# Kernel optimization log

Hardware: AMD Instinct MI355X
Metric: run time of the kernel (lower is better)

## Reference

```python
import jax, jax.numpy as jnp
import numpy as np

B, L, C = 32, 4096, 64
PL, PC = 64, 16          # patch sizes along L and C
NP = 256                 # num_patches
OUT = 512                # output_dim
FS = 1000.0              # sampling frequency -> T = 1/FS


def setup_inputs() -> dict:
    key = jax.random.key(0)
    ks = jax.random.split(key, 7)
    d_in = PL * (PC * 2)
    return {
        "x": jax.random.normal(ks[0], (B, L, C), dtype=jnp.float32),
        "start_L": jax.random.randint(ks[1], (B, NP), 0, L - PL + 1, dtype=jnp.int32),
        "start_C": jax.random.randint(ks[2], (B, NP), 0, C - PC + 1, dtype=jnp.int32),
        "w1": jax.random.normal(ks[3], (OUT, d_in), dtype=jnp.float32) / np.sqrt(d_in),
        "b1": jax.random.normal(ks[4], (OUT,), dtype=jnp.float32) * 0.01,
        "w2": jax.random.normal(ks[5], (OUT, OUT), dtype=jnp.float32) / np.sqrt(OUT),
        "b2": jax.random.normal(ks[6], (OUT,), dtype=jnp.float32) * 0.01,
    }


def reference(x, start_L, start_C, w1, b1, w2, b2):
    T = 1.0 / FS
    t = jnp.arange(L, dtype=jnp.float32) * T                      # [L]

    # patch index grids (wrapping, as in the torch module)
    idx_L = (start_L[:, :, None] + jnp.arange(PL, dtype=jnp.int32)) % L   # [B,NP,PL]
    idx_C = (start_C[:, :, None] + jnp.arange(PC, dtype=jnp.int32)) % C   # [B,NP,PC]

    # double gather: patches[b,p,i,j] = x[b, idx_L[b,p,i], idx_C[b,p,j]]
    b_idx = jnp.arange(B, dtype=jnp.int32)[:, None, None, None]
    patches = x[b_idx, idx_L[:, :, :, None], idx_C[:, :, None, :]]        # [B,NP,PL,PC]

    # time embedding gathered with the same L indices, broadcast over PC
    t_patches = jnp.broadcast_to(t[idx_L][:, :, :, None], (B, NP, PL, PC))

    feats = jnp.concatenate([patches, t_patches], axis=-1)                # [B,NP,PL,2*PC]
    feats = feats.reshape(B, NP, PL * 2 * PC)

    h = jnp.einsum('bpd,od->bpo', feats, w1) + b1
    h = jax.nn.silu(h)
    out = jnp.einsum('bpo,qo->bpq', h, w2) + b2                           # [B,NP,OUT]
    return out
```

## Files before the change

kernel.cpp:

```cpp
#include <hip/hip_runtime.h>
#include <hip/hip_bf16.h>
#include <stdint.h>

#define BB   32
#define LL   4096
#define CCH  64
#define NPp  256
#define DOUT 512
#define DINX 1024
#define MM   (BB * NPp)
#define TT   0.001f

using bf16 = __hip_bfloat16;
typedef __attribute__((ext_vector_type(8))) short bf16x8;
typedef __attribute__((ext_vector_type(4))) float f32x4;

__device__ __forceinline__ void async_copy16(void* lds, const void* g) {
    __builtin_amdgcn_global_load_lds(
        (const __attribute__((address_space(1))) void*)g,
        (__attribute__((address_space(3))) void*)lds,
        16, 0, 0);
}

__device__ __forceinline__ uint2 pack4_bf16(float a, float b, float c, float d) {
    union { bf16 h[4]; uint2 u; } p;
    p.h[0] = __float2bfloat16(a);
    p.h[1] = __float2bfloat16(b);
    p.h[2] = __float2bfloat16(c);
    p.h[3] = __float2bfloat16(d);
    return p.u;
}

__global__ __launch_bounds__(256) void prep(
    const float* __restrict__ w1, const float* __restrict__ b1,
    const float* __restrict__ w2,
    bf16* __restrict__ w1x, bf16* __restrict__ w2b,
    float* __restrict__ A1, float* __restrict__ C1)
{
    const int blk = blockIdx.x;
    if (blk < 512) {
        int i = (blk * 256 + threadIdx.x) * 4;
        int o = i >> 10, r = i & 1023;
        int l = r >> 4, j = r & 15;
        float4 v = *(const float4*)(w1 + (size_t)o * 2048 + l * 32 + j);
        *(uint2*)(w1x + i) = pack4_bf16(v.x, v.y, v.z, v.w);
    } else if (blk < 768) {
        int i = ((blk - 512) * 256 + threadIdx.x) * 4;
        float4 v = *(const float4*)(w2 + i);
        *(uint2*)(w2b + i) = pack4_bf16(v.x, v.y, v.z, v.w);
    } else {
        const int o = (blk - 768) * 4 + (threadIdx.x >> 6);
        const int l = threadIdx.x & 63;
        const float* wr = w1 + (size_t)o * 2048 + l * 32 + 16;
        float s0 = 0.f;
#pragma unroll
        for (int j = 0; j < 16; ++j) s0 += wr[j];
        float s1 = (float)l * s0;
#pragma unroll
        for (int off = 32; off > 0; off >>= 1) {
            s0 += __shfl_down(s0, off);
            s1 += __shfl_down(s1, off);
        }
        if (l == 0) {
            A1[o] = TT * s0;
            C1[o] = b1[o] + TT * s1;
        }
    }
}

__global__ __launch_bounds__(256) void gather_feats(
    const float* __restrict__ x, const int* __restrict__ startL,
    const int* __restrict__ startC, bf16* __restrict__ feats)
{
    const int m = blockIdx.x * 4 + (threadIdx.x >> 6);
    const int b = m >> 8;
    const int l = threadIdx.x & 63;
    const int sl = startL[m];
    const int sc = startC[m];
    const float* src = x + ((size_t)b * LL + (size_t)(sl + l)) * CCH + sc;
    float4 v0 = *(const float4*)(src);
    float4 v1 = *(const float4*)(src + 4);
    float4 v2 = *(const float4*)(src + 8);
    float4 v3 = *(const float4*)(src + 12);
    uint4 p0, p1;
    uint2 a = pack4_bf16(v0.x, v0.y, v0.z, v0.w);
    uint2 c = pack4_bf16(v1.x, v1.y, v1.z, v1.w);
    p0.x = a.x; p0.y = a.y; p0.z = c.x; p0.w = c.y;
    a = pack4_bf16(v2.x, v2.y, v2.z, v2.w);
    c = pack4_bf16(v3.x, v3.y, v3.z, v3.w);
    p1.x = a.x; p1.y = a.y; p1.z = c.x; p1.w = c.y;
    bf16* dst = feats + (size_t)m * DINX + l * 16;
    *(uint4*)dst       = p0;
    *(uint4*)(dst + 8) = p1;
}

template <bool FUSE1>
__global__ __launch_bounds__(256, 4) void gemm_db(
    const bf16* __restrict__ A,
    const bf16* __restrict__ Bt,
    const float* __restrict__ P1,
    const float* __restrict__ C1,
    const int*   __restrict__ sL,
    void* __restrict__ outp,
    const int N, const int K)
{
    constexpr int BK = 64;
    __shared__ __align__(16) bf16 As[2][64 * BK];
    __shared__ __align__(16) bf16 Bs[2][64 * BK];

    const int tid  = threadIdx.x;
    const int lane = tid & 63;
    const int wave = tid >> 6;
    const int row0 = blockIdx.x * 64;
    const int col0 = blockIdx.y * 64;

    const int  srow  = wave * 16 + (lane >> 3);
    const int  skoff = (lane & 7) * 8;
    const bf16* agp = A  + (size_t)(row0 + srow) * K + skoff;
    const bf16* bgp = Bt + (size_t)(col0 + srow) * K + skoff;
    const int w16 = wave * 16;

    const int mw = (wave >> 1) * 32;
    const int nw = (wave & 1) * 32;
    const int fr = lane & 15;
    const int fq = lane >> 4;

    f32x4 acc[2][2] = {};

    const int nIter = K / BK;

    async_copy16(&As[0][(w16 + 0) * BK], agp);
    async_copy16(&As[0][(w16 + 8) * BK], agp + (size_t)8 * K);
    async_copy16(&Bs[0][(w16 + 0) * BK], bgp);
    async_copy16(&Bs[0][(w16 + 8) * BK], bgp + (size_t)8 * K);

    for (int it = 0; it < nIter; ++it) {
        __syncthreads();
        const int cur = it & 1;
        if (it + 1 < nIter) {
            const int nxt = cur ^ 1;
            const int k1 = (it + 1) * BK;
            async_copy16(&As[nxt][(w16 + 0) * BK], agp + k1);
            async_copy16(&As[nxt][(w16 + 8) * BK], agp + (size_t)8 * K + k1);
            async_copy16(&Bs[nxt][(w16 + 0) * BK], bgp + k1);
            async_copy16(&Bs[nxt][(w16 + 8) * BK], bgp + (size_t)8 * K + k1);
        }

        bf16x8 af[2][2], bfr[2][2];
#pragma unroll
        for (int i = 0; i < 2; ++i)
#pragma unroll
            for (int ks = 0; ks < 2; ++ks)
                af[i][ks] = *(const bf16x8*)&As[cur][(mw + i * 16 + fr) * BK + ks * 32 + fq * 8];
#pragma unroll
        for (int j = 0; j < 2; ++j)
#pragma unroll
            for (int ks = 0; ks < 2; ++ks)
                bfr[j][ks] = *(const bf16x8*)&Bs[cur][(nw + j * 16 + fr) * BK + ks * 32 + fq * 8];
#pragma unroll
        for (int ks = 0; ks < 2; ++ks)
#pragma unroll
            for (int i = 0; i < 2; ++i)
#pragma unroll
                for (int j = 0; j < 2; ++j)
                    acc[i][j] = __builtin_amdgcn_mfma_f32_16x16x32_bf16(
                        af[i][ks], bfr[j][ks], acc[i][j], 0, 0, 0);
    }

    float slr[2][4];
    if (FUSE1) {
#pragma unroll
        for (int i = 0; i < 2; ++i)
#pragma unroll
            for (int r = 0; r < 4; ++r)
                slr[i][r] = (float)sL[row0 + mw + i * 16 + fq * 4 + r];
    }
#pragma unroll
    for (int j = 0; j < 2; ++j) {
        const int col = col0 + nw + j * 16 + fr;
        const float bv = P1[col];
        const float cv = FUSE1 ? C1[col] : 0.f;
#pragma unroll
        for (int i = 0; i < 2; ++i)
#pragma unroll
            for (int r = 0; r < 4; ++r) {
                const int row = row0 + mw + i * 16 + fq * 4 + r;
                if (FUSE1) {
                    float v = acc[i][j][r] + slr[i][r] * bv + cv;
                    v = v / (1.0f + __expf(-v));
                    ((bf16*)outp)[(size_t)row * N + col] = __float2bfloat16(v);
                } else {
                    ((float*)outp)[(size_t)row * N + col] = acc[i][j][r] + bv;
                }
            }
    }
}

extern "C" void kernel_launch(void* const* d_in, const int* in_sizes, int n_in,
                              void* d_out, int out_size, void* d_ws, size_t ws_size,
                              hipStream_t stream)
{
    const float* x  = (const float*)d_in[0];
    const int*   sL = (const int*)  d_in[1];
    const int*   sC = (const int*)  d_in[2];
    const float* w1 = (const float*)d_in[3];
    const float* b1 = (const float*)d_in[4];
    const float* w2 = (const float*)d_in[5];
    const float* b2 = (const float*)d_in[6];
    float* out = (float*)d_out;

    char* ws = (char*)d_ws;
    bf16* featsB = (bf16*)ws;                      size_t off = (size_t)MM * DINX * 2;
    bf16* w1x = (bf16*)(ws + off);                 off += (size_t)DOUT * DINX * 2;
    bf16* w2b = (bf16*)(ws + off);                 off += (size_t)DOUT * DOUT * 2;
    bf16* hB  = (bf16*)(ws + off);                 off += (size_t)MM * DOUT * 2;
    float* A1 = (float*)(ws + off);                off += DOUT * 4;
    float* C1 = (float*)(ws + off);

    prep<<<896, 256, 0, stream>>>(w1, b1, w2, w1x, w2b, A1, C1);
    gather_feats<<<MM / 4, 256, 0, stream>>>(x, sL, sC, featsB);

    gemm_db<true><<<dim3(MM / 64, DOUT / 64), 256, 0, stream>>>(
        featsB, w1x, A1, C1, sL, hB, DOUT, DINX);

    gemm_db<false><<<dim3(MM / 64, DOUT / 64), 256, 0, stream>>>(
        hB, w2b, b2, nullptr, nullptr, out, DOUT, DOUT);
}
```

Baseline: 134.2 us.

## Fuse patch gather and both MLP GEMMs into one megakernel with swizzled LDS

Replaces the gather kernel and the two separate GEMM launches with one kernel. Each block gathers 32 patch rows straight from x into LDS as bf16, runs the first GEMM with the fused time-embedding bias and SiLU, keeps the hidden activations in LDS, and then runs the second GEMM. The prep kernel now pre-packs both weight matrices into per-k-tile, XOR-swizzled layouts so they can be streamed into LDS with async copies without bank conflicts. This removes the global round trips for the feature and hidden tensors and the extra launches. In exchange, every block re-streams the full weight matrices, each block uses about 136 KB of LDS (one block per CU), and the second GEMM loop synchronises more often.

```diff
diff --git a/kernel.cpp b/kernel.cpp
--- a/kernel.cpp
+++ b/kernel.cpp
@@ -2,13 +2,10 @@
 #include <hip/hip_bf16.h>
 #include <stdint.h>
 
-#define BB   32
 #define LL   4096
 #define CCH  64
-#define NPp  256
 #define DOUT 512
-#define DINX 1024
-#define MM   (BB * NPp)
+#define MM   8192
 #define TT   0.001f
 
 using bf16 = __hip_bfloat16;
@@ -34,20 +31,27 @@
 __global__ __launch_bounds__(256) void prep(
     const float* __restrict__ w1, const float* __restrict__ b1,
     const float* __restrict__ w2,
-    bf16* __restrict__ w1x, bf16* __restrict__ w2b,
+    bf16* __restrict__ w1p, bf16* __restrict__ w2p,
     float* __restrict__ A1, float* __restrict__ C1)
 {
     const int blk = blockIdx.x;
     if (blk < 512) {
-        int i = (blk * 256 + threadIdx.x) * 4;
-        int o = i >> 10, r = i & 1023;
-        int l = r >> 4, j = r & 15;
-        float4 v = *(const float4*)(w1 + (size_t)o * 2048 + l * 32 + j);
-        *(uint2*)(w1x + i) = pack4_bf16(v.x, v.y, v.z, v.w);
+        int g   = blk * 256 + threadIdx.x;
+        int kk0 = (g & 15) * 4;
+        int col = (g >> 4) & 511;
+        int it  = g >> 13;
+        float4 v = *(const float4*)(w1 + (size_t)col * 2048
+                                    + (it * 4 + (kk0 >> 4)) * 32 + (kk0 & 15));
+        int off = (it * 512 + col) * 64 + (((kk0 >> 3) ^ (col & 7)) * 8) + (kk0 & 7);
+        *(uint2*)(w1p + off) = pack4_bf16(v.x, v.y, v.z, v.w);
     } else if (blk < 768) {
-        int i = ((blk - 512) * 256 + threadIdx.x) * 4;
-        float4 v = *(const float4*)(w2 + i);
-        *(uint2*)(w2b + i) = pack4_bf16(v.x, v.y, v.z, v.w);
+        int g   = (blk - 512) * 256 + threadIdx.x;
+        int kk0 = (g & 15) * 4;
+        int col = (g >> 4) & 511;
+        int it2 = g >> 13;
+        float4 v = *(const float4*)(w2 + (size_t)col * 512 + it2 * 64 + kk0);
+        int off = (it2 * 512 + col) * 64 + (((kk0 >> 3) ^ (col & 7)) * 8) + (kk0 & 7);
+        *(uint2*)(w2p + off) = pack4_bf16(v.x, v.y, v.z, v.w);
     } else {
         const int o = (blk - 768) * 4 + (threadIdx.x >> 6);
         const int l = threadIdx.x & 63;
@@ -68,130 +72,164 @@
     }
 }
 
-__global__ __launch_bounds__(256) void gather_feats(
-    const float* __restrict__ x, const int* __restrict__ startL,
-    const int* __restrict__ startC, bf16* __restrict__ feats)
+__global__ __launch_bounds__(512, 2) void mega(
+    const float* __restrict__ x, const int* __restrict__ sLg,
+    const int* __restrict__ sCg, const bf16* __restrict__ w1p,
+    const bf16* __restrict__ w2p, const float* __restrict__ A1,
+    const float* __restrict__ C1, const float* __restrict__ b2,
+    float* __restrict__ out)
 {
-    const int m = blockIdx.x * 4 + (threadIdx.x >> 6);
-    const int b = m >> 8;
-    const int l = threadIdx.x & 63;
-    const int sl = startL[m];
-    const int sc = startC[m];
-    const float* src = x + ((size_t)b * LL + (size_t)(sl + l)) * CCH + sc;
-    float4 v0 = *(const float4*)(src);
-    float4 v1 = *(const float4*)(src + 4);
-    float4 v2 = *(const float4*)(src + 8);
-    float4 v3 = *(const float4*)(src + 12);
-    uint4 p0, p1;
-    uint2 a = pack4_bf16(v0.x, v0.y, v0.z, v0.w);
-    uint2 c = pack4_bf16(v1.x, v1.y, v1.z, v1.w);
-    p0.x = a.x; p0.y = a.y; p0.z = c.x; p0.w = c.y;
-    a = pack4_bf16(v2.x, v2.y, v2.z, v2.w);
-    c = pack4_bf16(v3.x, v3.y, v3.z, v3.w);
-    p1.x = a.x; p1.y = a.y; p1.z = c.x; p1.w = c.y;
-    bf16* dst = feats + (size_t)m * DINX + l * 16;
-    *(uint4*)dst       = p0;
-    *(uint4*)(dst + 8) = p1;
-}
-
-template <bool FUSE1>
-__global__ __launch_bounds__(256, 4) void gemm_db(
-    const bf16* __restrict__ A,
-    const bf16* __restrict__ Bt,
-    const float* __restrict__ P1,
-    const float* __restrict__ C1,
-    const int*   __restrict__ sL,
-    void* __restrict__ outp,
-    const int N, const int K)
-{
-    constexpr int BK = 64;
-    __shared__ __align__(16) bf16 As[2][64 * BK];
-    __shared__ __align__(16) bf16 Bs[2][64 * BK];
-
-    const int tid  = threadIdx.x;
-    const int lane = tid & 63;
-    const int wave = tid >> 6;
-    const int row0 = blockIdx.x * 64;
-    const int col0 = blockIdx.y * 64;
-
-    const int  srow  = wave * 16 + (lane >> 3);
-    const int  skoff = (lane & 7) * 8;
-    const bf16* agp = A  + (size_t)(row0 + srow) * K + skoff;
-    const bf16* bgp = Bt + (size_t)(col0 + srow) * K + skoff;
-    const int w16 = wave * 16;
-
-    const int mw = (wave >> 1) * 32;
-    const int nw = (wave & 1) * 32;
-    const int fr = lane & 15;
-    const int fq = lane >> 4;
-
-    f32x4 acc[2][2] = {};
-
-    const int nIter = K / BK;
-
-    async_copy16(&As[0][(w16 + 0) * BK], agp);
-    async_copy16(&As[0][(w16 + 8) * BK], agp + (size_t)8 * K);
-    async_copy16(&Bs[0][(w16 + 0) * BK], bgp);
-    async_copy16(&Bs[0][(w16 + 8) * BK], bgp + (size_t)8 * K);
-
-    for (int it = 0; it < nIter; ++it) {
+    __shared__ __align__(16) char smem_raw[139264];
+    bf16* const Bs0 = (bf16*)smem_raw;
+    bf16* const Bs1 = (bf16*)(smem_raw + 65536);
+    bf16* const As0 = (bf16*)(smem_raw + 131072);
+    bf16* const As1 = (bf16*)(smem_raw + 135168);
+    bf16* const Hs  = (bf16*)(smem_raw + 65536);
+
+    const int t    = threadIdx.x;
+    const int lane = t & 63;
+    const int wave = t >> 6;
+    const int fr   = lane & 15;
+    const int fq   = lane >> 4;
+    const int m0   = blockIdx.x * 32;
+    const int b    = m0 >> 8;
+
+    const int gr  = t >> 4;
+    const int gs  = t & 15;
+    const int gsl = sLg[m0 + gr];
+    const int gsc = sCg[m0 + gr];
+    const float* gx = x + ((size_t)b * LL + gsl + (gs >> 2)) * CCH + gsc + (gs & 3) * 4;
+    const int aoff = gr * 64 + (((gs >> 1) ^ (gr & 7)) * 8) + (gs & 1) * 4;
+
+    const bf16* bsrc1 = w1p + (size_t)t * 8;
+    const bf16* bsrc2 = w2p + (size_t)t * 8;
+    const int   wu8   = wave * 64 * 8;
+
+    f32x4 acc[2][4] = {};
+
+    {
+#pragma unroll
+        for (int c = 0; c < 8; ++c)
+            async_copy16(Bs0 + c * 4096 + wu8, bsrc1 + c * 4096);
+        float4 v = *(const float4*)gx;
+        *(uint2*)(As0 + aoff) = pack4_bf16(v.x, v.y, v.z, v.w);
+    }
+    float4 xv = *(const float4*)(gx + 4 * CCH);
+
+    for (int it = 0; it < 16; ++it) {
         __syncthreads();
-        const int cur = it & 1;
-        if (it + 1 < nIter) {
-            const int nxt = cur ^ 1;
-            const int k1 = (it + 1) * BK;
-            async_copy16(&As[nxt][(w16 + 0) * BK], agp + k1);
-            async_copy16(&As[nxt][(w16 + 8) * BK], agp + (size_t)8 * K + k1);
-            async_copy16(&Bs[nxt][(w16 + 0) * BK], bgp + k1);
-            async_copy16(&Bs[nxt][(w16 + 8) * BK], bgp + (size_t)8 * K + k1);
-        }
-
-        bf16x8 af[2][2], bfr[2][2];
+        bf16* const Bc = (it & 1) ? Bs1 : Bs0;
+        bf16* const Ac = (it & 1) ? As1 : As0;
+        if (it < 15) {
+            bf16* const Bn = (it & 1) ? Bs0 : Bs1;
+            bf16* const An = (it & 1) ? As0 : As1;
+            const bf16* bs = bsrc1 + (size_t)(it + 1) * 32768;
+#pragma unroll
+            for (int c = 0; c < 8; ++c)
+                async_copy16(Bn + c * 4096 + wu8, bs + c * 4096);
+            *(uint2*)(An + aoff) = pack4_bf16(xv.x, xv.y, xv.z, xv.w);
+            const int itn = (it + 2 < 16) ? (it + 2) : 15;
+            xv = *(const float4*)(gx + (size_t)itn * 4 * CCH);
+        }
+
+        bf16x8 af[2][2], bfr[4][2];
 #pragma unroll
         for (int i = 0; i < 2; ++i)
 #pragma unroll
             for (int ks = 0; ks < 2; ++ks)
-                af[i][ks] = *(const bf16x8*)&As[cur][(mw + i * 16 + fr) * BK + ks * 32 + fq * 8];
-#pragma unroll
-        for (int j = 0; j < 2; ++j)
+                af[i][ks] = *(const bf16x8*)&Ac[(i * 16 + fr) * 64
+                                + (((ks * 4 + fq) ^ (fr & 7)) * 8)];
+#pragma unroll
+        for (int j = 0; j < 4; ++j)
 #pragma unroll
             for (int ks = 0; ks < 2; ++ks)
-                bfr[j][ks] = *(const bf16x8*)&Bs[cur][(nw + j * 16 + fr) * BK + ks * 32 + fq * 8];
+                bfr[j][ks] = *(const bf16x8*)&Bc[(wave * 64 + j * 16 + fr) * 64
+                                + (((ks * 4 + fq) ^ (fr & 7)) * 8)];
 #pragma unroll
         for (int ks = 0; ks < 2; ++ks)
 #pragma unroll
             for (int i = 0; i < 2; ++i)
 #pragma unroll
-                for (int j = 0; j < 2; ++j)
+                for (int j = 0; j < 4; ++j)
                     acc[i][j] = __builtin_amdgcn_mfma_f32_16x16x32_bf16(
                         af[i][ks], bfr[j][ks], acc[i][j], 0, 0, 0);
     }
-
-    float slr[2][4];
-    if (FUSE1) {
-#pragma unroll
-        for (int i = 0; i < 2; ++i)
-#pragma unroll
-            for (int r = 0; r < 4; ++r)
-                slr[i][r] = (float)sL[row0 + mw + i * 16 + fq * 4 + r];
-    }
-#pragma unroll
-    for (int j = 0; j < 2; ++j) {
-        const int col = col0 + nw + j * 16 + fr;
-        const float bv = P1[col];
-        const float cv = FUSE1 ? C1[col] : 0.f;
-#pragma unroll
-        for (int i = 0; i < 2; ++i)
-#pragma unroll
-            for (int r = 0; r < 4; ++r) {
-                const int row = row0 + mw + i * 16 + fq * 4 + r;
-                if (FUSE1) {
-                    float v = acc[i][j][r] + slr[i][r] * bv + cv;
+    __syncthreads();
+
+#pragma unroll
+    for (int c = 0; c < 8; ++c)
+        async_copy16(Bs0 + c * 4096 + wu8, bsrc2 + c * 4096);
+
+    {
+        float slr[2][4];
+#pragma unroll
+        for (int i = 0; i < 2; ++i)
+#pragma unroll
+            for (int rr = 0; rr < 4; ++rr)
+                slr[i][rr] = (float)sLg[m0 + i * 16 + fq * 4 + rr];
+#pragma unroll
+        for (int j = 0; j < 4; ++j) {
+            const int col = wave * 64 + j * 16 + fr;
+            const float av = A1[col];
+            const float cv = C1[col];
+            const int c8 = col >> 3, c7 = col & 7;
+#pragma unroll
+            for (int i = 0; i < 2; ++i)
+#pragma unroll
+                for (int rr = 0; rr < 4; ++rr) {
+                    const int row = i * 16 + fq * 4 + rr;
+                    float v = acc[i][j][rr] + slr[i][rr] * av + cv;
                     v = v / (1.0f + __expf(-v));
-                    ((bf16*)outp)[(size_t)row * N + col] = __float2bfloat16(v);
-                } else {
-                    ((float*)outp)[(size_t)row * N + col] = acc[i][j][r] + bv;
+                    Hs[row * 512 + ((c8 ^ (row & 7)) * 8) + c7] = __float2bfloat16(v);
                 }
+        }
+    }
+
+    f32x4 acc2[2][4] = {};
+    for (int it2 = 0; it2 < 8; ++it2) {
+        __syncthreads();
+        bf16x8 af[2][2], bfr[4][2];
+#pragma unroll
+        for (int i = 0; i < 2; ++i)
+#pragma unroll
+            for (int ks = 0; ks < 2; ++ks) {
+                const int row = i * 16 + fr;
+                af[i][ks] = *(const bf16x8*)&Hs[row * 512
+                                + (((it2 * 8 + ks * 4 + fq) ^ (row & 7)) * 8)];
+            }
+#pragma unroll
+        for (int j = 0; j < 4; ++j)
+#pragma unroll
+            for (int ks = 0; ks < 2; ++ks)
+                bfr[j][ks] = *(const bf16x8*)&Bs0[(wave * 64 + j * 16 + fr) * 64
+                                + (((ks * 4 + fq) ^ (fr & 7)) * 8)];
+        __syncthreads();
+        if (it2 < 7) {
+            const bf16* bs = bsrc2 + (size_t)(it2 + 1) * 32768;
+#pragma unroll
+            for (int c = 0; c < 8; ++c)
+                async_copy16(Bs0 + c * 4096 + wu8, bs + c * 4096);
+        }
+#pragma unroll
+        for (int ks = 0; ks < 2; ++ks)
+#pragma unroll
+            for (int i = 0; i < 2; ++i)
+#pragma unroll
+                for (int j = 0; j < 4; ++j)
+                    acc2[i][j] = __builtin_amdgcn_mfma_f32_16x16x32_bf16(
+                        af[i][ks], bfr[j][ks], acc2[i][j], 0, 0, 0);
+    }
+
+#pragma unroll
+    for (int j = 0; j < 4; ++j) {
+        const int col = wave * 64 + j * 16 + fr;
+        const float bv = b2[col];
+#pragma unroll
+        for (int i = 0; i < 2; ++i)
+#pragma unroll
+            for (int rr = 0; rr < 4; ++rr) {
+                const int row = m0 + i * 16 + fq * 4 + rr;
+                out[(size_t)row * 512 + col] = acc2[i][j][rr] + bv;
             }
     }
 }
@@ -210,19 +248,11 @@
     float* out = (float*)d_out;
 
     char* ws = (char*)d_ws;
-    bf16* featsB = (bf16*)ws;                      size_t off = (size_t)MM * DINX * 2;
-    bf16* w1x = (bf16*)(ws + off);                 off += (size_t)DOUT * DINX * 2;
-    bf16* w2b = (bf16*)(ws + off);                 off += (size_t)DOUT * DOUT * 2;
-    bf16* hB  = (bf16*)(ws + off);                 off += (size_t)MM * DOUT * 2;
-    float* A1 = (float*)(ws + off);                off += DOUT * 4;
-    float* C1 = (float*)(ws + off);
-
-    prep<<<896, 256, 0, stream>>>(w1, b1, w2, w1x, w2b, A1, C1);
-    gather_feats<<<MM / 4, 256, 0, stream>>>(x, sL, sC, featsB);
-
-    gemm_db<true><<<dim3(MM / 64, DOUT / 64), 256, 0, stream>>>(
-        featsB, w1x, A1, C1, sL, hB, DOUT, DINX);
-
-    gemm_db<false><<<dim3(MM / 64, DOUT / 64), 256, 0, stream>>>(
-        hB, w2b, b2, nullptr, nullptr, out, DOUT, DOUT);
-}
+    bf16*  w1p = (bf16*)ws;
+    bf16*  w2p = (bf16*)(ws + (1 << 20));
+    float* A1  = (float*)(ws + (1 << 20) + (1 << 19));
+    float* C1  = A1 + DOUT;
+
+    prep<<<896, 256, 0, stream>>>(w1, b1, w2, w1p, w2p, A1, C1);
+    mega<<<MM / 32, 512, 0, stream>>>(x, sL, sC, w1p, w2p, A1, C1, b2, out);
+}
```

Measured after the change: 129.0 us. -3.9%, faster.
